# Kernel tuning notes

Hardware: AMD Instinct MI355X
Metric: run time of the kernel (lower is better)

The kernel has to match this reference:

```python
import jax, jax.numpy as jnp
import numpy as np

N, G, E = 100000, 32768, 1000000
F, H = 64, 64


def _mlp(x, w1, b1, w2, b2):
    # Linear -> SiLU -> Linear (matches nn.Sequential in the torch module)
    return jax.nn.silu(x @ w1 + b1) @ w2 + b2


def setup_inputs() -> dict:
    key = jax.random.key(0)
    ks = jax.random.split(key, 24)

    def lin(k, fan_in, fan_out):
        s = 1.0 / np.sqrt(fan_in)
        kw, kb = jax.random.split(k)
        w = jax.random.uniform(kw, (fan_in, fan_out), jnp.float32, -s, s)
        b = jax.random.uniform(kb, (fan_out,), jnp.float32, -s, s)
        return w, b

    node_w1, node_b1 = lin(ks[0], F, H)
    node_w2, node_b2 = lin(ks[1], H, H)
    edge_w1, edge_b1 = lin(ks[2], 6, H)
    edge_w2, edge_b2 = lin(ks[3], H, H)
    msg_w1, msg_b1 = lin(ks[4], 2 * H, H)
    msg_w2, msg_b2 = lin(ks[5], H, H)
    upd_w1, upd_b1 = lin(ks[6], H, H)
    upd_w2, upd_b2 = lin(ks[7], H, H)

    return {
        "node_features": jax.random.normal(ks[8], (N, F), jnp.float32),
        "node_pos": jax.random.normal(ks[9], (N, 3), jnp.float32),
        "grid_pos": jax.random.normal(ks[10], (G, 3), jnp.float32),
        "orientations": jax.random.normal(ks[11], (N, 3, 3), jnp.float32),
        "edge_index": jnp.stack([
            jax.random.randint(ks[12], (E,), 0, N),
            jax.random.randint(ks[13], (E,), 0, G),
        ]),
        "node_w1": node_w1, "node_b1": node_b1, "node_w2": node_w2, "node_b2": node_b2,
        "edge_w1": edge_w1, "edge_b1": edge_b1, "edge_w2": edge_w2, "edge_b2": edge_b2,
        "msg_w1": msg_w1, "msg_b1": msg_b1, "msg_w2": msg_w2, "msg_b2": msg_b2,
        "upd_w1": upd_w1, "upd_b1": upd_b1, "upd_w2": upd_w2, "upd_b2": upd_b2,
    }


def reference(node_features, node_pos, grid_pos, orientations, edge_index,
              node_w1, node_b1, node_w2, node_b2,
              edge_w1, edge_b1, edge_w2, edge_b2,
              msg_w1, msg_b1, msg_w2, msg_b2,
              upd_w1, upd_b1, upd_w2, upd_b2):
    source, target = edge_index[0], edge_index[1]
    num_grid = grid_pos.shape[0]

    # node MLP
    h_node = _mlp(node_features, node_w1, node_b1, node_w2, node_b2)  # [N,H]

    # per-edge message with orientation-aware projection
    pos_s = node_pos[source]                 # [E,3]
    rel = grid_pos[target] - pos_s           # [E,3]
    # bmm(rel[:,None,:], R[source]).squeeze(1) == einsum ei,eij->ej
    trel = jnp.einsum("ei,eij->ej", rel, orientations[source])
    edge_attr = jnp.concatenate([pos_s, trel], axis=-1)        # [E,6]
    e_feat = _mlp(edge_attr, edge_w1, edge_b1, edge_w2, edge_b2)
    msg_in = jnp.concatenate([h_node[source], e_feat], axis=-1)  # [E,2H]
    messages = _mlp(msg_in, msg_w1, msg_b1, msg_w2, msg_b2)      # [E,H]

    # scatter-mean into grid buckets (mask out-of-range targets)
    valid = (target >= 0) & (target < num_grid)
    idx = jnp.where(valid, target, 0)
    msg_masked = jnp.where(valid[:, None], messages, 0.0)
    sums = jax.ops.segment_sum(msg_masked, idx, num_segments=num_grid)
    cnts = jax.ops.segment_sum(valid.astype(jnp.float32), idx, num_segments=num_grid)
    grid_feat = sums / jnp.maximum(cnts, 1.0)[:, None]

    return _mlp(grid_feat, upd_w1, upd_b1, upd_w2, upd_b2)  # [G,H]
```

## Files before the change

kernel.cpp:

```cpp
#include <hip/hip_runtime.h>
#include <hip/hip_bf16.h>
#include <cstdint>

typedef __attribute__((ext_vector_type(8))) short short8;
typedef __attribute__((ext_vector_type(4))) float f32x4;
typedef unsigned short u16;

__device__ __forceinline__ float b2f(u16 u) {
  union { unsigned int i; float f; } v; v.i = ((unsigned int)u) << 16; return v.f;
}
__device__ __forceinline__ u16 f2b(float f) {
  __hip_bfloat16 h = __float2bfloat16(f);
  union { __hip_bfloat16 h; u16 u; } v; v.h = h; return v.u;
}
__device__ __forceinline__ float silu_f(float x) { return x / (1.0f + __expf(-x)); }

__device__ __forceinline__ float loadF(const void* p, long i, int isf32) {
  if (isf32) return ((const float*)p)[i];
  return b2f(((const u16*)p)[i]);
}

__device__ __forceinline__ int sniffbit(u16 u) {
  unsigned e = (u >> 7) & 0xffu;
  return (e >= 0xC0u || (e < 0x40u && (u & 0x7fffu) != 0)) ? 1 : 0;
}

struct Ptrs { const void* p[20]; int n[20]; };

#define FW_EW1 0
#define FW_UW1 384
#define FW_UW2 4480
#define FW_UB1 8576
#define FW_UB2 8640
#define FW_EB1 8704
#define FW_EB2 8768
#define FW_MB1 8832
#define FW_MB2 8896
#define FW_TOTAL 8960

#define IMG_EW2 0
#define IMG_MW1 4608
#define IMG_MW2 13312
#define IMG_TOTAL 17920

#define PREP_BLOCKS 105
#define HIST_BLOCKS 1024

__global__ __launch_bounds__(256) void detect_k(Ptrs a, int* flags) {
  int j = blockIdx.x;
  const u16* q = (const u16*)a.p[j];
  int n = a.n[j];
  int m = n < 4096 ? n : 4096;
  int cnt = 0;
  for (int i = threadIdx.x; i < m; i += 256) cnt += sniffbit(q[i]);
  __shared__ int tot;
  if (threadIdx.x == 0) tot = 0;
  __syncthreads();
  if (cnt) atomicAdd(&tot, cnt);
  __syncthreads();
  if (threadIdx.x == 0) flags[j] = (tot >= 2) ? 1 : 0;
}

__global__ __launch_bounds__(256) void fused_a(
    Ptrs a, const int* __restrict__ flags,
    u16* __restrict__ img, float* __restrict__ fw,
    const int* __restrict__ eidx, int* __restrict__ cnt8,
    u16* __restrict__ hout, int nrows, long E, int G)
{
  const int t = threadIdx.x;
  const int b = blockIdx.x;

  if (b < HIST_BLOCKS) {
    int* cs = cnt8 + (size_t)(b & 7) * G;
    long i = (long)b * 256 + t;
    const long stride = (long)HIST_BLOCKS * 256;
    for (; i < E; i += stride) {
      int tg = eidx[E + i];
      if (tg >= 0 && tg < G) atomicAdd(&cs[tg], 1);
    }
    return;
  }

  if (b < HIST_BLOCKS + PREP_BLOCKS) {
    int i = (b - HIST_BLOCKS) * 256 + t;
    if (i < IMG_TOTAL) {
      const void* bp; int fl; long si; bool real;
      if (i < IMG_MW1) { int nn = i / 72, k = i % 72; bp = a.p[10]; fl = flags[10]; real = k < 64; si = (long)k * 64 + nn; }
      else if (i < IMG_MW2) { int t2 = i - IMG_MW1; int nn = t2 / 136, k = t2 % 136; bp = a.p[12]; fl = flags[12]; real = k < 128; si = (long)k * 64 + nn; }
      else { int t2 = i - IMG_MW2; int nn = t2 / 72, k = t2 % 72; bp = a.p[14]; fl = flags[14]; real = k < 64; si = (long)k * 64 + nn; }
      u16 val = 0;
      if (real) val = f2b(loadF(bp, si, fl));
      img[i] = val;
    } else if (i < IMG_TOTAL + FW_TOTAL) {
      int j = i - IMG_TOTAL;
      const void* bp; int fl; long si;
      if (j < 384)        { bp = a.p[8];  fl = flags[8];  si = j; }
      else if (j < 4480)  { bp = a.p[16]; fl = flags[16]; si = j - 384; }
      else if (j < 8576)  { bp = a.p[18]; fl = flags[18]; si = j - 4480; }
      else {
        int bb = j - 8576; int seg = bb >> 6; si = bb & 63;
        switch (seg) {
          case 0: bp = a.p[17]; fl = flags[17]; break;
          case 1: bp = a.p[19]; fl = flags[19]; break;
          case 2: bp = a.p[9];  fl = flags[9];  break;
          case 3: bp = a.p[11]; fl = flags[11]; break;
          case 4: bp = a.p[13]; fl = flags[13]; break;
          default: bp = a.p[15]; fl = flags[15]; break;
        }
      }
      fw[j] = loadF(bp, si, fl);
    }
    return;
  }

  __shared__ float xs[64][68];
  __shared__ float w1s[64][68];
  __shared__ float w2s[64][68];
  __shared__ float b1s[64];
  __shared__ float b2s[64];
  const void* x = a.p[0];
  const int xf = flags[0], f1 = flags[4], fb1 = flags[5], f2 = flags[6], fb2 = flags[7];
  const long rbase = (long)(b - HIST_BLOCKS - PREP_BLOCKS) * 64;
  for (int i = t; i < 4096; i += 256) {
    int k = i >> 6, cc = i & 63;
    w1s[k][cc] = loadF(a.p[4], i, f1);
    w2s[k][cc] = loadF(a.p[6], i, f2);
  }
  if (t < 64) { b1s[t] = loadF(a.p[5], t, fb1); b2s[t] = loadF(a.p[7], t, fb2); }
  {
    int row = t >> 2, ch = t & 3;
    long rg = rbase + row;
    if (rg < nrows) {
      if (xf) {
        const float* xp = (const float*)x + rg * 64 + ch * 16;
#pragma unroll
        for (int m = 0; m < 16; ++m) xs[row][ch * 16 + m] = xp[m];
      } else {
        const u16* xp = (const u16*)x + rg * 64 + ch * 16;
#pragma unroll
        for (int m = 0; m < 16; ++m) xs[row][ch * 16 + m] = b2f(xp[m]);
      }
    } else {
#pragma unroll
      for (int m = 0; m < 16; ++m) xs[row][ch * 16 + m] = 0.f;
    }
  }
  __syncthreads();
  const int r0 = (t >> 4) * 4, c0 = (t & 15) * 4;
  float acc[4][4];
#pragma unroll
  for (int i = 0; i < 4; ++i)
#pragma unroll
    for (int j = 0; j < 4; ++j) acc[i][j] = b1s[c0 + j];
  for (int k = 0; k < 64; ++k) {
    float w0 = w1s[k][c0], w1v = w1s[k][c0 + 1], w2v = w1s[k][c0 + 2], w3v = w1s[k][c0 + 3];
#pragma unroll
    for (int i = 0; i < 4; ++i) {
      float av = xs[r0 + i][k];
      acc[i][0] = fmaf(av, w0, acc[i][0]);
      acc[i][1] = fmaf(av, w1v, acc[i][1]);
      acc[i][2] = fmaf(av, w2v, acc[i][2]);
      acc[i][3] = fmaf(av, w3v, acc[i][3]);
    }
  }
  __syncthreads();
#pragma unroll
  for (int i = 0; i < 4; ++i)
#pragma unroll
    for (int j = 0; j < 4; ++j) xs[r0 + i][c0 + j] = silu_f(acc[i][j]);
  __syncthreads();
  float acc2[4][4];
#pragma unroll
  for (int i = 0; i < 4; ++i)
#pragma unroll
    for (int j = 0; j < 4; ++j) acc2[i][j] = b2s[c0 + j];
  for (int k = 0; k < 64; ++k) {
    float w0 = w2s[k][c0], w1v = w2s[k][c0 + 1], w2v = w2s[k][c0 + 2], w3v = w2s[k][c0 + 3];
#pragma unroll
    for (int i = 0; i < 4; ++i) {
      float av = xs[r0 + i][k];
      acc2[i][0] = fmaf(av, w0, acc2[i][0]);
      acc2[i][1] = fmaf(av, w1v, acc2[i][1]);
      acc2[i][2] = fmaf(av, w2v, acc2[i][2]);
      acc2[i][3] = fmaf(av, w3v, acc2[i][3]);
    }
  }
#pragma unroll
  for (int i = 0; i < 4; ++i) {
    long rg = rbase + r0 + i;
    if (rg < nrows) {
#pragma unroll
      for (int j = 0; j < 4; ++j) hout[rg * 64 + c0 + j] = f2b(acc2[i][j]);
    }
  }
}

__global__ __launch_bounds__(256) void scan_k(const int* __restrict__ cnt8,
                                              int* __restrict__ cursor8,
                                              int* __restrict__ bsum, int G) {
  __shared__ int sd[256];
  const int t = threadIdx.x;
  const long tot = 8L * G;
  long j0 = (long)blockIdx.x * 1024 + (long)t * 4;
  int v[4];
#pragma unroll
  for (int k = 0; k < 4; ++k) {
    long j = j0 + k;
    v[k] = (j < tot) ? cnt8[(size_t)(j & 7) * G + (j >> 3)] : 0;
  }
  int local = v[0] + v[1] + v[2] + v[3];
  sd[t] = local;
  __syncthreads();
  for (int off = 1; off < 256; off <<= 1) {
    int x2 = (t >= off) ? sd[t - off] : 0;
    __syncthreads();
    sd[t] += x2;
    __syncthreads();
  }
  int p = sd[t] - local;
#pragma unroll
  for (int k = 0; k < 4; ++k) {
    long j = j0 + k;
    if (j < tot) cursor8[(size_t)(j & 7) * G + (j >> 3)] = p;
    p += v[k];
  }
  if (t == 255) bsum[blockIdx.x] = sd[255];
}

__global__ __launch_bounds__(256) void scat_k(const int* __restrict__ eidx,
                                              int* __restrict__ cursor8,
                                              const int* __restrict__ bsum,
                                              unsigned int* __restrict__ pkS,
                                              int* __restrict__ evp,
                                              long E, int G, int NB2) {
  __shared__ int bo[256];
  const int t = threadIdx.x;
  int v = (t < NB2) ? bsum[t] : 0;
  bo[t] = v;
  __syncthreads();
  for (int off = 1; off < 256; off <<= 1) {
    int x2 = (t >= off) ? bo[t - off] : 0;
    __syncthreads();
    bo[t] += x2;
    __syncthreads();
  }
  if (blockIdx.x == 0 && t == 0) *evp = bo[NB2 - 1];
  int excl = bo[t] - v;
  __syncthreads();
  bo[t] = excl;
  __syncthreads();
  const int c = blockIdx.x & 7;
  int* cur = cursor8 + (size_t)c * G;
  long i = (long)blockIdx.x * 256 + t;
  const long stride = (long)gridDim.x * 256;
  for (; i < E; i += stride) {
    int tg = eidx[E + i];
    if (tg >= 0 && tg < G) {
      int s = eidx[i];
      long j = ((long)tg << 3) | c;
      int p = atomicAdd(&cur[tg], 1) + bo[j >> 10];
      __builtin_nontemporal_store((unsigned int)s | ((unsigned int)tg << 17), pkS + p);
    }
  }
}

#define ETILES 4

__global__ __launch_bounds__(256, 5) void edge_kernel(
    const void* node_pos, const void* grid_pos, const void* orient,
    const unsigned int* __restrict__ pkS, const int* __restrict__ evp,
    const u16* __restrict__ h_node, const u16* __restrict__ img,
    const float* __restrict__ fw, const int* __restrict__ flags,
    float* __restrict__ sums, int G)
{
  __shared__ __align__(16) u16 hA[64][136];
  __shared__ __align__(16) u16 ef1[64][72];
  __shared__ float eaf[64][6];
  __shared__ float w1e[6][64];
  __shared__ float biasE[4][64];
  __shared__ int tgt_s[64];
  float (*msgf)[66] = (float (*)[66])&hA[0][0];

  const int t = threadIdx.x;
  const int pf = flags[1], gf = flags[2], of = flags[3];
  const int Ev = *evp;
  for (int i = t; i < 384; i += 256) w1e[i / 64][i % 64] = fw[FW_EW1 + i];
  { int seg = t >> 6, cc = t & 63; biasE[seg][cc] = fw[FW_EB1 + seg * 64 + cc]; }
  __syncthreads();

  const int lane = t & 63, w = t >> 6;
  const int q = lane >> 4, c = lane & 15;
  const int m0 = w * 16;
  const u16* wE2 = img + IMG_EW2;
  const u16* wM1 = img + IMG_MW1;
  const u16* wM2 = img + IMG_MW2;
  const f32x4 z = {0.f, 0.f, 0.f, 0.f};

  for (int tile = 0; tile < ETILES; ++tile) {
    long base = ((long)blockIdx.x * ETILES + tile) * 64;
    if (base >= Ev) break;
    if (t < 64) {
      long eg = base + t;
      int s = 0, tg = -1;
      if (eg < Ev) {
        unsigned int pk = pkS[eg];
        s = (int)(pk & 0x1FFFFu);
        tg = (int)(pk >> 17);
      }
      tgt_s[t] = tg;
      int tgc = (tg >= 0) ? tg : 0;
      float ps[3], rel[3], tr[3];
#pragma unroll
      for (int i = 0; i < 3; ++i) {
        ps[i] = loadF(node_pos, (long)s * 3 + i, pf);
        rel[i] = loadF(grid_pos, (long)tgc * 3 + i, gf) - ps[i];
      }
#pragma unroll
      for (int j = 0; j < 3; ++j) tr[j] = 0.f;
#pragma unroll
      for (int i = 0; i < 3; ++i)
#pragma unroll
        for (int j = 0; j < 3; ++j)
          tr[j] = fmaf(rel[i], loadF(orient, (long)s * 9 + i * 3 + j, of), tr[j]);
      eaf[t][0] = ps[0]; eaf[t][1] = ps[1]; eaf[t][2] = ps[2];
      eaf[t][3] = tr[0]; eaf[t][4] = tr[1]; eaf[t][5] = tr[2];
    }
    {
      int e = t >> 2, ch = t & 3;
      long eg = base + e;
      int s = 0;
      if (eg < Ev) s = (int)(pkS[eg] & 0x1FFFFu);
      const u16* hp = h_node + (long)s * 64 + ch * 16;
      short8 v0 = *(const short8*)hp;
      short8 v1 = *(const short8*)(hp + 8);
      *(short8*)&hA[e][ch * 16] = v0;
      *(short8*)&hA[e][ch * 16 + 8] = v1;
    }
    __syncthreads();

    {
      int e = t >> 2, c0 = (t & 3) * 16;
      float a0 = eaf[e][0], a1 = eaf[e][1], a2 = eaf[e][2];
      float a3 = eaf[e][3], a4 = eaf[e][4], a5 = eaf[e][5];
      __align__(16) u16 tmp[16];
#pragma unroll
      for (int j = 0; j < 16; ++j) {
        int cc = c0 + j;
        float acc = biasE[0][cc];
        acc = fmaf(a0, w1e[0][cc], acc);
        acc = fmaf(a1, w1e[1][cc], acc);
        acc = fmaf(a2, w1e[2][cc], acc);
        acc = fmaf(a3, w1e[3][cc], acc);
        acc = fmaf(a4, w1e[4][cc], acc);
        acc = fmaf(a5, w1e[5][cc], acc);
        tmp[j] = f2b(silu_f(acc));
      }
      *(short8*)&ef1[e][c0] = *(const short8*)tmp;
      *(short8*)&ef1[e][c0 + 8] = *(const short8*)(tmp + 8);
    }
    __syncthreads();
    {
      short8 a0 = *(const short8*)&ef1[m0 + c][q * 8];
      short8 a1 = *(const short8*)&ef1[m0 + c][32 + q * 8];
#pragma unroll
      for (int nt = 0; nt < 4; ++nt) {
        short8 b0 = *(const short8*)&wE2[(nt * 16 + c) * 72 + q * 8];
        short8 b1v = *(const short8*)&wE2[(nt * 16 + c) * 72 + 32 + q * 8];
        f32x4 acc = __builtin_amdgcn_mfma_f32_16x16x32_bf16(a0, b0, z, 0, 0, 0);
        acc = __builtin_amdgcn_mfma_f32_16x16x32_bf16(a1, b1v, acc, 0, 0, 0);
#pragma unroll
        for (int r = 0; r < 4; ++r) {
          int row = m0 + q * 4 + r, col = nt * 16 + c;
          hA[row][64 + col] = f2b(acc[r] + biasE[1][col]);
        }
      }
    }
    __syncthreads();
    {
      short8 a0 = *(const short8*)&hA[m0 + c][q * 8];
      short8 a1 = *(const short8*)&hA[m0 + c][32 + q * 8];
      short8 a2 = *(const short8*)&hA[m0 + c][64 + q * 8];
      short8 a3 = *(const short8*)&hA[m0 + c][96 + q * 8];
#pragma unroll
      for (int nt = 0; nt < 4; ++nt) {
        const u16* wp = &wM1[(nt * 16 + c) * 136];
        f32x4 acc = __builtin_amdgcn_mfma_f32_16x16x32_bf16(a0, *(const short8*)(wp + q * 8), z, 0, 0, 0);
        acc = __builtin_amdgcn_mfma_f32_16x16x32_bf16(a1, *(const short8*)(wp + 32 + q * 8), acc, 0, 0, 0);
        acc = __builtin_amdgcn_mfma_f32_16x16x32_bf16(a2, *(const short8*)(wp + 64 + q * 8), acc, 0, 0, 0);
        acc = __builtin_amdgcn_mfma_f32_16x16x32_bf16(a3, *(const short8*)(wp + 96 + q * 8), acc, 0, 0, 0);
#pragma unroll
        for (int r = 0; r < 4; ++r) {
          int row = m0 + q * 4 + r, col = nt * 16 + c;
          ef1[row][col] = f2b(silu_f(acc[r] + biasE[2][col]));
        }
      }
    }
    __syncthreads();
    {
      short8 a0 = *(const short8*)&ef1[m0 + c][q * 8];
      short8 a1 = *(const short8*)&ef1[m0 + c][32 + q * 8];
#pragma unroll
      for (int nt = 0; nt < 4; ++nt) {
        short8 b0 = *(const short8*)&wM2[(nt * 16 + c) * 72 + q * 8];
        short8 b1v = *(const short8*)&wM2[(nt * 16 + c) * 72 + 32 + q * 8];
        f32x4 acc = __builtin_amdgcn_mfma_f32_16x16x32_bf16(a0, b0, z, 0, 0, 0);
        acc = __builtin_amdgcn_mfma_f32_16x16x32_bf16(a1, b1v, acc, 0, 0, 0);
#pragma unroll
        for (int r = 0; r < 4; ++r) {
          int row = m0 + q * 4 + r, col = nt * 16 + c;
          msgf[row][col] = acc[r] + biasE[3][col];
        }
      }
    }
    __syncthreads();
    {
      int col = lane;
      int r0 = w * 16;
      int cur = tgt_s[r0];
      float run = msgf[r0][col];
      bool lopen = (r0 == 0) ? true : (tgt_s[r0 - 1] == cur);
#pragma unroll
      for (int r2 = 1; r2 < 16; ++r2) {
        int r = r0 + r2;
        int tg = tgt_s[r];
        float v = msgf[r][col];
        if (tg == cur) {
          run += v;
        } else {
          if (cur >= 0) {
            if (lopen) unsafeAtomicAdd(&sums[(long)cur * 64 + col], run);
            else sums[(long)cur * 64 + col] = run;
          }
          cur = tg; run = v; lopen = false;
        }
      }
      bool ropen = (r0 + 16 >= 64) ? true : (tgt_s[r0 + 16] == cur);
      if (cur >= 0) {
        if (lopen || ropen) unsafeAtomicAdd(&sums[(long)cur * 64 + col], run);
        else sums[(long)cur * 64 + col] = run;
      }
    }
    __syncthreads();
  }
}

__global__ __launch_bounds__(256) void upd_mlp(
    const float* __restrict__ sums, const int* __restrict__ cnt8,
    const float* __restrict__ fw, float* __restrict__ out, int nrows)
{
  __shared__ float xs[64][68];
  __shared__ float w1s[64][68];
  __shared__ float w2s[64][68];
  __shared__ float b1s[64];
  __shared__ float b2s[64];
  const int t = threadIdx.x;
  const long rbase = (long)blockIdx.x * 64;
  for (int i = t; i < 4096; i += 256) {
    int k = i >> 6, cc = i & 63;
    w1s[k][cc] = fw[FW_UW1 + i];
    w2s[k][cc] = fw[FW_UW2 + i];
  }
  if (t < 64) { b1s[t] = fw[FW_UB1 + t]; b2s[t] = fw[FW_UB2 + t]; }
  {
    int row = t >> 2, ch = t & 3;
    long rg = rbase + row;
    if (rg < nrows) {
      int cn = 0;
#pragma unroll
      for (int cc = 0; cc < 8; ++cc) cn += cnt8[(size_t)cc * nrows + rg];
      float inv = 1.0f / fmaxf((float)cn, 1.0f);
      const float* p = sums + rg * 64 + ch * 16;
#pragma unroll
      for (int m = 0; m < 16; ++m) xs[row][ch * 16 + m] = p[m] * inv;
    } else {
#pragma unroll
      for (int m = 0; m < 16; ++m) xs[row][ch * 16 + m] = 0.f;
    }
  }
  __syncthreads();
  const int r0 = (t >> 4) * 4, c0 = (t & 15) * 4;
  float acc[4][4];
#pragma unroll
  for (int i = 0; i < 4; ++i)
#pragma unroll
    for (int j = 0; j < 4; ++j) acc[i][j] = b1s[c0 + j];
  for (int k = 0; k < 64; ++k) {
    float w0 = w1s[k][c0], w1v = w1s[k][c0 + 1], w2v = w1s[k][c0 + 2], w3v = w1s[k][c0 + 3];
#pragma unroll
    for (int i = 0; i < 4; ++i) {
      float av = xs[r0 + i][k];
      acc[i][0] = fmaf(av, w0, acc[i][0]);
      acc[i][1] = fmaf(av, w1v, acc[i][1]);
      acc[i][2] = fmaf(av, w2v, acc[i][2]);
      acc[i][3] = fmaf(av, w3v, acc[i][3]);
    }
  }
  __syncthreads();
#pragma unroll
  for (int i = 0; i < 4; ++i)
#pragma unroll
    for (int j = 0; j < 4; ++j) xs[r0 + i][c0 + j] = silu_f(acc[i][j]);
  __syncthreads();
  float acc2[4][4];
#pragma unroll
  for (int i = 0; i < 4; ++i)
#pragma unroll
    for (int j = 0; j < 4; ++j) acc2[i][j] = b2s[c0 + j];
  for (int k = 0; k < 64; ++k) {
    float w0 = w2s[k][c0], w1v = w2s[k][c0 + 1], w2v = w2s[k][c0 + 2], w3v = w2s[k][c0 + 3];
#pragma unroll
    for (int i = 0; i < 4; ++i) {
      float av = xs[r0 + i][k];
      acc2[i][0] = fmaf(av, w0, acc2[i][0]);
      acc2[i][1] = fmaf(av, w1v, acc2[i][1]);
      acc2[i][2] = fmaf(av, w2v, acc2[i][2]);
      acc2[i][3] = fmaf(av, w3v, acc2[i][3]);
    }
  }
#pragma unroll
  for (int i = 0; i < 4; ++i) {
    long rg = rbase + r0 + i;
    if (rg < nrows) {
#pragma unroll
      for (int j = 0; j < 4; ++j) out[rg * 64 + c0 + j] = acc2[i][j];
    }
  }
}

extern "C" void kernel_launch(void* const* d_in, const int* in_sizes, int n_in,
                              void* d_out, int out_size, void* d_ws, size_t ws_size,
                              hipStream_t stream) {
  const int N = in_sizes[1] / 3;
  const int G = in_sizes[2] / 3;
  const long E = (long)in_sizes[4] / 2;
  const int NB2 = (int)((8L * G + 1023) / 1024);
  const int nodeBlocks = (N + 63) / 64;

  char* ws = (char*)d_ws;
  float* sums = (float*)ws;
  size_t off = (size_t)G * 256;
  int* cnt8 = (int*)(ws + off);     off += (size_t)G * 32;
  int* cursor8 = (int*)(ws + off);  off += (size_t)G * 32;
  int* bsum = (int*)(ws + off);     off += 1024;
  int* evp = (int*)(ws + off);      off += 256;
  int* flags = (int*)(ws + off);    off += 256;
  unsigned int* pkS = (unsigned int*)(ws + off); off += (size_t)E * 4;
  u16* h_node = (u16*)(ws + off);   off += (size_t)N * 128;
  u16* img = (u16*)(ws + off);      off += (size_t)IMG_TOTAL * 2;
  float* fw = (float*)(ws + off);

  hipMemsetAsync(ws, 0, (size_t)G * 288, stream);

  Ptrs a;
  const int map[20] = {0,1,2,3, 5,6,7,8, 9,10,11,12, 13,14,15,16, 17,18,19,20};
  for (int i = 0; i < 20; ++i) { a.p[i] = d_in[map[i]]; a.n[i] = in_sizes[map[i]]; }

  detect_k<<<20, 256, 0, stream>>>(a, flags);
  fused_a<<<HIST_BLOCKS + PREP_BLOCKS + nodeBlocks, 256, 0, stream>>>(
      a, flags, img, fw, (const int*)d_in[4], cnt8, h_node, N, E, G);
  scan_k<<<NB2, 256, 0, stream>>>(cnt8, cursor8, bsum, G);
  scat_k<<<1024, 256, 0, stream>>>((const int*)d_in[4], cursor8, bsum, pkS, evp, E, G, NB2);
  edge_kernel<<<(int)((E + ETILES * 64 - 1) / (ETILES * 64)), 256, 0, stream>>>(
      d_in[1], d_in[2], d_in[3], pkS, evp, h_node, img, fw, flags, sums, G);
  upd_mlp<<<(G + 63) / 64, 256, 0, stream>>>(sums, cnt8, fw, (float*)d_out, G);
}
```

Baseline: 463.5 us.

## Regroup launches and shrink edge kernel shared memory with per-wave buffers

```diff
diff --git a/kernel.cpp b/kernel.cpp
--- a/kernel.cpp
+++ b/kernel.cpp
@@ -46,30 +46,12 @@
 #define PREP_BLOCKS 105
 #define HIST_BLOCKS 1024
 
-__global__ __launch_bounds__(256) void detect_k(Ptrs a, int* flags) {
-  int j = blockIdx.x;
-  const u16* q = (const u16*)a.p[j];
-  int n = a.n[j];
-  int m = n < 4096 ? n : 4096;
-  int cnt = 0;
-  for (int i = threadIdx.x; i < m; i += 256) cnt += sniffbit(q[i]);
-  __shared__ int tot;
-  if (threadIdx.x == 0) tot = 0;
-  __syncthreads();
-  if (cnt) atomicAdd(&tot, cnt);
-  __syncthreads();
-  if (threadIdx.x == 0) flags[j] = (tot >= 2) ? 1 : 0;
-}
-
-__global__ __launch_bounds__(256) void fused_a(
-    Ptrs a, const int* __restrict__ flags,
-    u16* __restrict__ img, float* __restrict__ fw,
-    const int* __restrict__ eidx, int* __restrict__ cnt8,
-    u16* __restrict__ hout, int nrows, long E, int G)
+__global__ __launch_bounds__(256) void hist_detect_k(
+    Ptrs a, const int* __restrict__ eidx, int* __restrict__ cnt8,
+    int* __restrict__ flags, long E, int G)
 {
   const int t = threadIdx.x;
   const int b = blockIdx.x;
-
   if (b < HIST_BLOCKS) {
     int* cs = cnt8 + (size_t)(b & 7) * G;
     long i = (long)b * 256 + t;
@@ -80,9 +62,62 @@
     }
     return;
   }
-
-  if (b < HIST_BLOCKS + PREP_BLOCKS) {
-    int i = (b - HIST_BLOCKS) * 256 + t;
+  int j = b - HIST_BLOCKS;
+  const u16* q = (const u16*)a.p[j];
+  int n = a.n[j];
+  int m = n < 4096 ? n : 4096;
+  int cnt = 0;
+  for (int i = t; i < m; i += 256) cnt += sniffbit(q[i]);
+  __shared__ int tot;
+  if (t == 0) tot = 0;
+  __syncthreads();
+  if (cnt) atomicAdd(&tot, cnt);
+  __syncthreads();
+  if (t == 0) flags[j] = (tot >= 2) ? 1 : 0;
+}
+
+__global__ __launch_bounds__(256) void scan_prep_node_k(
+    Ptrs a, const int* __restrict__ flags,
+    const int* __restrict__ cnt8, int* __restrict__ cursor8,
+    int* __restrict__ bsum,
+    u16* __restrict__ img, float* __restrict__ fw,
+    u16* __restrict__ hout, int nrows, int G, int NB2)
+{
+  const int t = threadIdx.x;
+  const int b = blockIdx.x;
+
+  if (b < NB2) {
+    __shared__ int sd[256];
+    const long tot = 8L * G;
+    long j0 = (long)b * 1024 + (long)t * 4;
+    int v[4];
+#pragma unroll
+    for (int k = 0; k < 4; ++k) {
+      long j = j0 + k;
+      v[k] = (j < tot) ? cnt8[(size_t)(j & 7) * G + (j >> 3)] : 0;
+    }
+    int local = v[0] + v[1] + v[2] + v[3];
+    sd[t] = local;
+    __syncthreads();
+    for (int off = 1; off < 256; off <<= 1) {
+      int x2 = (t >= off) ? sd[t - off] : 0;
+      __syncthreads();
+      sd[t] += x2;
+      __syncthreads();
+    }
+    int p = sd[t] - local;
+#pragma unroll
+    for (int k = 0; k < 4; ++k) {
+      long j = j0 + k;
+      if (j < tot) cursor8[(size_t)(j & 7) * G + (j >> 3)] = p;
+      p += v[k];
+    }
+    if (t == 255) bsum[b] = sd[255];
+    return;
+  }
+
+  if (b < NB2 + PREP_BLOCKS) {
+    int i = (b - NB2) * 256 + t;
     if (i < IMG_TOTAL) {
       const void* bp; int fl; long si; bool real;
       if (i < IMG_MW1) { int nn = i / 72, k = i % 72; bp = a.p[10]; fl = flags[10]; real = k < 64; si = (long)k * 64 + nn; }
@@ -120,7 +155,7 @@
   __shared__ float b2s[64];
   const void* x = a.p[0];
   const int xf = flags[0], f1 = flags[4], fb1 = flags[5], f2 = flags[6], fb2 = flags[7];
-  const long rbase = (long)(b - HIST_BLOCKS - PREP_BLOCKS) * 64;
+  const long rbase = (long)(b - NB2 - PREP_BLOCKS) * 64;
   for (int i = t; i < 4096; i += 256) {
     int k = i >> 6, cc = i & 63;
     w1s[k][cc] = loadF(a.p[4], i, f1);
@@ -193,38 +228,6 @@
       for (int j = 0; j < 4; ++j) hout[rg * 64 + c0 + j] = f2b(acc2[i][j]);
     }
   }
-}
-
-__global__ __launch_bounds__(256) void scan_k(const int* __restrict__ cnt8,
-                                              int* __restrict__ cursor8,
-                                              int* __restrict__ bsum, int G) {
-  __shared__ int sd[256];
-  const int t = threadIdx.x;
-  const long tot = 8L * G;
-  long j0 = (long)blockIdx.x * 1024 + (long)t * 4;
-  int v[4];
-#pragma unroll
-  for (int k = 0; k < 4; ++k) {
-    long j = j0 + k;
-    v[k] = (j < tot) ? cnt8[(size_t)(j & 7) * G + (j >> 3)] : 0;
-  }
-  int local = v[0] + v[1] + v[2] + v[3];
-  sd[t] = local;
-  __syncthreads();
-  for (int off = 1; off < 256; off <<= 1) {
-    int x2 = (t >= off) ? sd[t - off] : 0;
-    __syncthreads();
-    sd[t] += x2;
-    __syncthreads();
-  }
-  int p = sd[t] - local;
-#pragma unroll
-  for (int k = 0; k < 4; ++k) {
-    long j = j0 + k;
-    if (j < tot) cursor8[(size_t)(j & 7) * G + (j >> 3)] = p;
-    p += v[k];
-  }
-  if (t == 255) bsum[blockIdx.x] = sd[255];
 }
 
 __global__ __launch_bounds__(256) void scat_k(const int* __restrict__ eidx,
@@ -266,20 +269,19 @@
 
 #define ETILES 4
 
-__global__ __launch_bounds__(256, 5) void edge_kernel(
+__global__ __launch_bounds__(256, 7) void edge_kernel(
     const void* node_pos, const void* grid_pos, const void* orient,
     const unsigned int* __restrict__ pkS, const int* __restrict__ evp,
     const u16* __restrict__ h_node, const u16* __restrict__ img,
     const float* __restrict__ fw, const int* __restrict__ flags,
     float* __restrict__ sums, int G)
 {
-  __shared__ __align__(16) u16 hA[64][136];
-  __shared__ __align__(16) u16 ef1[64][72];
+  __shared__ __align__(16) u16 pool[4][2304];
   __shared__ float eaf[64][6];
   __shared__ float w1e[6][64];
   __shared__ float biasE[4][64];
   __shared__ int tgt_s[64];
-  float (*msgf)[66] = (float (*)[66])&hA[0][0];
+  __shared__ int src_s[64];
 
   const int t = threadIdx.x;
   const int pf = flags[1], gf = flags[2], of = flags[3];
@@ -291,6 +293,9 @@
   const int lane = t & 63, w = t >> 6;
   const int q = lane >> 4, c = lane & 15;
   const int m0 = w * 16;
+  u16 (* __restrict__ ef1w)[72] = (u16 (*)[72])&pool[w][0];
+  u16 (* __restrict__ hAw)[72]  = (u16 (*)[72])&pool[w][1152];
+  float (* __restrict__ msgfw)[66] = (float (*)[66])&pool[w][0];
   const u16* wE2 = img + IMG_EW2;
   const u16* wM1 = img + IMG_MW1;
   const u16* wM2 = img + IMG_MW2;
@@ -299,15 +304,17 @@
   for (int tile = 0; tile < ETILES; ++tile) {
     long base = ((long)blockIdx.x * ETILES + tile) * 64;
     if (base >= Ev) break;
-    if (t < 64) {
-      long eg = base + t;
+    __syncthreads();
+    if (lane < 16) {
+      long eg = base + m0 + lane;
       int s = 0, tg = -1;
       if (eg < Ev) {
         unsigned int pk = pkS[eg];
         s = (int)(pk & 0x1FFFFu);
         tg = (int)(pk >> 17);
       }
-      tgt_s[t] = tg;
+      tgt_s[m0 + lane] = tg;
+      src_s[m0 + lane] = s;
       int tgc = (tg >= 0) ? tg : 0;
       float ps[3], rel[3], tr[3];
 #pragma unroll
@@ -322,26 +329,17 @@
 #pragma unroll
         for (int j = 0; j < 3; ++j)
           tr[j] = fmaf(rel[i], loadF(orient, (long)s * 9 + i * 3 + j, of), tr[j]);
-      eaf[t][0] = ps[0]; eaf[t][1] = ps[1]; eaf[t][2] = ps[2];
-      eaf[t][3] = tr[0]; eaf[t][4] = tr[1]; eaf[t][5] = tr[2];
-    }
+      eaf[m0 + lane][0] = ps[0]; eaf[m0 + lane][1] = ps[1]; eaf[m0 + lane][2] = ps[2];
+      eaf[m0 + lane][3] = tr[0]; eaf[m0 + lane][4] = tr[1]; eaf[m0 + lane][5] = tr[2];
+    }
+    __syncthreads();
+
     {
-      int e = t >> 2, ch = t & 3;
-      long eg = base + e;
-      int s = 0;
-      if (eg < Ev) s = (int)(pkS[eg] & 0x1FFFFu);
-      const u16* hp = h_node + (long)s * 64 + ch * 16;
-      short8 v0 = *(const short8*)hp;
-      short8 v1 = *(const short8*)(hp + 8);
-      *(short8*)&hA[e][ch * 16] = v0;
-      *(short8*)&hA[e][ch * 16 + 8] = v1;
-    }
-    __syncthreads();
-
-    {
-      int e = t >> 2, c0 = (t & 3) * 16;
-      float a0 = eaf[e][0], a1 = eaf[e][1], a2 = eaf[e][2];
-      float a3 = eaf[e][3], a4 = eaf[e][4], a5 = eaf[e][5];
+      int e = lane >> 2;
+      int eb = m0 + e;
+      int c0 = (lane & 3) * 16;
+      float a0 = eaf[eb][0], a1 = eaf[eb][1], a2 = eaf[eb][2];
+      float a3 = eaf[eb][3], a4 = eaf[eb][4], a5 = eaf[eb][5];
       __align__(16) u16 tmp[16];
 #pragma unroll
       for (int j = 0; j < 16; ++j) {
@@ -355,13 +353,13 @@
         acc = fmaf(a5, w1e[5][cc], acc);
         tmp[j] = f2b(silu_f(acc));
       }
-      *(short8*)&ef1[e][c0] = *(const short8*)tmp;
-      *(short8*)&ef1[e][c0 + 8] = *(const short8*)(tmp + 8);
+      *(short8*)&ef1w[e][c0] = *(const short8*)tmp;
+      *(short8*)&ef1w[e][c0 + 8] = *(const short8*)(tmp + 8);
     }
     __syncthreads();
     {
-      short8 a0 = *(const short8*)&ef1[m0 + c][q * 8];
-      short8 a1 = *(const short8*)&ef1[m0 + c][32 + q * 8];
+      short8 a0 = *(const short8*)&ef1w[c][q * 8];
+      short8 a1 = *(const short8*)&ef1w[c][32 + q * 8];
 #pragma unroll
       for (int nt = 0; nt < 4; ++nt) {
         short8 b0 = *(const short8*)&wE2[(nt * 16 + c) * 72 + q * 8];
@@ -370,17 +368,18 @@
         acc = __builtin_amdgcn_mfma_f32_16x16x32_bf16(a1, b1v, acc, 0, 0, 0);
 #pragma unroll
         for (int r = 0; r < 4; ++r) {
-          int row = m0 + q * 4 + r, col = nt * 16 + c;
-          hA[row][64 + col] = f2b(acc[r] + biasE[1][col]);
+          int row = q * 4 + r, col = nt * 16 + c;
+          hAw[row][col] = f2b(acc[r] + biasE[1][col]);
         }
       }
     }
     __syncthreads();
     {
-      short8 a0 = *(const short8*)&hA[m0 + c][q * 8];
-      short8 a1 = *(const short8*)&hA[m0 + c][32 + q * 8];
-      short8 a2 = *(const short8*)&hA[m0 + c][64 + q * 8];
-      short8 a3 = *(const short8*)&hA[m0 + c][96 + q * 8];
+      const u16* hp = h_node + (long)src_s[m0 + c] * 64;
+      short8 a0 = *(const short8*)(hp + q * 8);
+      short8 a1 = *(const short8*)(hp + 32 + q * 8);
+      short8 a2 = *(const short8*)&hAw[c][q * 8];
+      short8 a3 = *(const short8*)&hAw[c][32 + q * 8];
 #pragma unroll
       for (int nt = 0; nt < 4; ++nt) {
         const u16* wp = &wM1[(nt * 16 + c) * 136];
@@ -390,15 +389,16 @@
         acc = __builtin_amdgcn_mfma_f32_16x16x32_bf16(a3, *(const short8*)(wp + 96 + q * 8), acc, 0, 0, 0);
 #pragma unroll
         for (int r = 0; r < 4; ++r) {
-          int row = m0 + q * 4 + r, col = nt * 16 + c;
-          ef1[row][col] = f2b(silu_f(acc[r] + biasE[2][col]));
+          int row = q * 4 + r, col = nt * 16 + c;
+          ef1w[row][col] = f2b(silu_f(acc[r] + biasE[2][col]));
         }
       }
     }
     __syncthreads();
     {
-      short8 a0 = *(const short8*)&ef1[m0 + c][q * 8];
-      short8 a1 = *(const short8*)&ef1[m0 + c][32 + q * 8];
+      short8 a0 = *(const short8*)&ef1w[c][q * 8];
+      short8 a1 = *(const short8*)&ef1w[c][32 + q * 8];
+      __builtin_amdgcn_wave_barrier();
 #pragma unroll
       for (int nt = 0; nt < 4; ++nt) {
         short8 b0 = *(const short8*)&wM2[(nt * 16 + c) * 72 + q * 8];
@@ -407,23 +407,21 @@
         acc = __builtin_amdgcn_mfma_f32_16x16x32_bf16(a1, b1v, acc, 0, 0, 0);
 #pragma unroll
         for (int r = 0; r < 4; ++r) {
-          int row = m0 + q * 4 + r, col = nt * 16 + c;
-          msgf[row][col] = acc[r] + biasE[3][col];
+          int row = q * 4 + r, col = nt * 16 + c;
+          msgfw[row][col] = acc[r] + biasE[3][col];
         }
       }
     }
-    __syncthreads();
+    __builtin_amdgcn_wave_barrier();
     {
       int col = lane;
-      int r0 = w * 16;
-      int cur = tgt_s[r0];
-      float run = msgf[r0][col];
-      bool lopen = (r0 == 0) ? true : (tgt_s[r0 - 1] == cur);
+      int cur = tgt_s[m0];
+      float run = msgfw[0][col];
+      bool lopen = (m0 == 0) ? true : (tgt_s[m0 - 1] == cur);
 #pragma unroll
       for (int r2 = 1; r2 < 16; ++r2) {
-        int r = r0 + r2;
-        int tg = tgt_s[r];
-        float v = msgf[r][col];
+        int tg = tgt_s[m0 + r2];
+        float v = msgfw[r2][col];
         if (tg == cur) {
           run += v;
         } else {
@@ -434,13 +432,12 @@
           cur = tg; run = v; lopen = false;
         }
       }
-      bool ropen = (r0 + 16 >= 64) ? true : (tgt_s[r0 + 16] == cur);
+      bool ropen = (m0 + 16 >= 64) ? true : (tgt_s[m0 + 16] == cur);
       if (cur >= 0) {
         if (lopen || ropen) unsafeAtomicAdd(&sums[(long)cur * 64 + col], run);
         else sums[(long)cur * 64 + col] = run;
       }
     }
-    __syncthreads();
   }
 }
 
@@ -555,10 +552,10 @@
   const int map[20] = {0,1,2,3, 5,6,7,8, 9,10,11,12, 13,14,15,16, 17,18,19,20};
   for (int i = 0; i < 20; ++i) { a.p[i] = d_in[map[i]]; a.n[i] = in_sizes[map[i]]; }
 
-  detect_k<<<20, 256, 0, stream>>>(a, flags);
-  fused_a<<<HIST_BLOCKS + PREP_BLOCKS + nodeBlocks, 256, 0, stream>>>(
-      a, flags, img, fw, (const int*)d_in[4], cnt8, h_node, N, E, G);
-  scan_k<<<NB2, 256, 0, stream>>>(cnt8, cursor8, bsum, G);
+  hist_detect_k<<<HIST_BLOCKS + 20, 256, 0, stream>>>(
+      a, (const int*)d_in[4], cnt8, flags, E, G);
+  scan_prep_node_k<<<NB2 + PREP_BLOCKS + nodeBlocks, 256, 0, stream>>>(
+      a, flags, cnt8, cursor8, bsum, img, fw, h_node, N, G, NB2);
   scat_k<<<1024, 256, 0, stream>>>((const int*)d_in[4], cursor8, bsum, pkS, evp, E, G, NB2);
   edge_kernel<<<(int)((E + ETILES * 64 - 1) / (ETILES * 64)), 256, 0, stream>>>(
       d_in[1], d_in[2], d_in[3], pkS, evp, h_node, img, fw, flags, sums, G);
```

Result: slower. 486.3 us (+4.9%).
